# Kernel tuning notes

Hardware: AMD Instinct MI355X
Metric: run time of the kernel (lower is better)

## Reference

```python
import jax, jax.numpy as jnp
import numpy as np

B, C, H_IMG, W_IMG = 16, 384, 56, 56
NUM_HEADS = 6
HEAD_DIM = C // NUM_HEADS
BN_EPS = 1e-5


def _bn(x, gamma, beta, mean, var):
    # x: [b, ch, n] or [b, ch, h, w]; per-channel affine normalization (eval-mode BatchNorm)
    shape = (1, -1) + (1,) * (x.ndim - 2)
    scale = (gamma / jnp.sqrt(var + BN_EPS)).reshape(shape)
    shift = (beta - mean * gamma / jnp.sqrt(var + BN_EPS)).reshape(shape)
    return x * scale + shift


def setup_inputs() -> dict:
    key = jax.random.key(0)
    ks = jax.random.split(key, 12)
    c2 = 2 * C
    return {
        "x": jax.random.normal(ks[0], (B, C, H_IMG, W_IMG), jnp.float32),
        "qk_w": jax.random.normal(ks[1], (c2, C // 2), jnp.float32) * 0.05,
        "qk_gamma": jax.random.uniform(ks[2], (c2,), jnp.float32, 0.5, 1.5),
        "qk_beta": jax.random.normal(ks[3], (c2,), jnp.float32) * 0.1,
        "qk_mean": jax.random.normal(ks[4], (c2,), jnp.float32) * 0.1,
        "qk_var": jax.random.uniform(ks[5], (c2,), jnp.float32, 0.5, 1.5),
        "pe_w": jax.random.normal(ks[6], (C, 1, 3, 3), jnp.float32) * 0.1,
        "pe_gamma": jax.random.uniform(ks[7], (C,), jnp.float32, 0.5, 1.5),
        "pe_beta": jax.random.normal(ks[8], (C,), jnp.float32) * 0.1,
        "pe_mean": jax.random.normal(ks[9], (C,), jnp.float32) * 0.1,
        "pe_var": jax.random.uniform(ks[10], (C,), jnp.float32, 0.5, 1.5),
    }


def reference(x, qk_w, qk_gamma, qk_beta, qk_mean, qk_var,
              pe_w, pe_gamma, pe_beta, pe_mean, pe_var):
    b, c, h, w = x.shape
    n = h * w
    s = n ** (-0.5)
    nh, hd = NUM_HEADS, HEAD_DIM

    # grouped (groups=2) 1x1 conv: out channels [0:c] from input [0:c/2], [c:2c] from [c/2:c]
    xg = x.reshape(b, 2, c // 2, n)                       # [b, 2, c/2, n]
    wg = qk_w.reshape(2, c, c // 2)                       # [group, out_per_group, in_per_group]
    qk = jnp.einsum('bgin,goi->bgon', xg, wg).reshape(b, 2 * c, n)
    qk = _bn(qk, qk_gamma, qk_beta, qk_mean, qk_var)
    qk = jax.nn.elu(qk) + 1.0

    qk = qk.reshape(b, 2, nh, hd, n)
    q, k = qk[:, 0], qk[:, 1]                             # [b, H, d, n]
    v = x.reshape(b, nh, hd, n)                           # [b, H, d, n]

    # kv = (k*s) @ (v^T * s): [b, H, d, d]
    kv = jnp.einsum('bhdn,bhen->bhde', k * s, v * s)
    # numerator: q^T @ kv -> [b, H, n, d]
    num = jnp.einsum('bhdn,bhde->bhne', q, kv)
    # denominator: q^T @ mean_n(k) -> [b, H, n]
    den = jnp.einsum('bhdn,bhd->bhn', q, k.mean(axis=-1)) + 1e-6
    attn = (num / den[..., None]).transpose(0, 1, 3, 2).reshape(b, c, h, w)

    # depthwise 3x3 conv positional encoding on v (= x) + BN
    pe = jax.lax.conv_general_dilated(
        x, pe_w, window_strides=(1, 1), padding=((1, 1), (1, 1)),
        feature_group_count=c, dimension_numbers=('NCHW', 'OIHW', 'NCHW'))
    pe = _bn(pe, pe_gamma, pe_beta, pe_mean, pe_var)

    return attn + pe
```

## Files before the change

kernel.cpp:

```cpp
#include <hip/hip_runtime.h>
#include <math.h>

#define N_SP 3136
#define BN_EPS 1e-5f

typedef __attribute__((ext_vector_type(8))) short short8;
typedef __attribute__((ext_vector_type(4))) float f32x4;

#define K_SZ    (16*384*N_SP)
#define QB_OFF  (K_SZ)
#define QB_SZ   (16*384*N_SP)
#define KVP_OFF (QB_OFF + QB_SZ)
#define KVP_SZ  (16*6*7*64*80)
#define KVF_OFF (KVP_OFF + KVP_SZ)
#define KVF_SZ  (16*6*64*64)
#define KM_OFF  (KVF_OFF + KVF_SZ)
#define KM_SZ   (16*6*64)
#define WH_OFF  (KM_OFF + KM_SZ)
#define WSPLIT_N (2*384*192)
#define PWS_OFF (WH_OFF + WSPLIT_N)
#define PSH_OFF (PWS_OFF + 384*9)

#define FSWZ(n) ((((n) >> 1) ^ ((n) >> 2)) & 7)

__device__ __forceinline__ void bsplit(float f, ushort& h, ushort& l) {
    uint u = __float_as_uint(f);
    uint hr = (u + 0x7FFFu + ((u >> 16) & 1u)) >> 16;
    h = (ushort)hr;
    float fh = __uint_as_float(hr << 16);
    float fl = f - fh;
    uint v = __float_as_uint(fl);
    l = (ushort)((v + 0x7FFFu + ((v >> 16) & 1u)) >> 16);
}

__global__ __launch_bounds__(256) void p0_prep(
    const float* __restrict__ qk_w, const float* __restrict__ pe_w,
    const float* __restrict__ pgamma, const float* __restrict__ pbeta,
    const float* __restrict__ pmean, const float* __restrict__ pvar,
    ushort* __restrict__ wh, ushort* __restrict__ wl,
    float* __restrict__ pwsc, float* __restrict__ psh)
{
    int idx = blockIdx.x * 256 + threadIdx.x;
    if (idx < WSPLIT_N) {
        ushort h, l;
        bsplit(qk_w[idx], h, l);
        wh[idx] = h;
        wl[idx] = l;
    }
    if (idx < 384) {
        float sc = pgamma[idx] / sqrtf(pvar[idx] + BN_EPS);
        psh[idx] = pbeta[idx] - pmean[idx] * sc;
        #pragma unroll
        for (int q = 0; q < 9; ++q) pwsc[idx * 9 + q] = pe_w[idx * 9 + q] * sc;
    }
}

__global__ __launch_bounds__(256) void k1_qk_mfma(
    const float* __restrict__ x, const ushort* __restrict__ wh, const ushort* __restrict__ wl,
    const float* __restrict__ gamma, const float* __restrict__ beta,
    const float* __restrict__ mean, const float* __restrict__ var,
    uint* __restrict__ kq, float* __restrict__ qbuf)
{
    __shared__ __align__(16) ushort Ah[8192];
    __shared__ __align__(16) ushort Al[8192];
    __shared__ __align__(16) ushort Bh[4096];
    __shared__ __align__(16) ushort Bl[4096];

    const int bx = blockIdx.x;
    const int by = blockIdx.y;
    const int bz = blockIdx.z;
    const int b = bz >> 1, gg = bz & 1;
    const int t = threadIdx.x;
    const int lane = t & 63, wv = t >> 6;
    const int wr = wv >> 1, wc = wv & 1;
    const int lg = lane >> 4, l15 = lane & 15;

    f32x4 acc[4][2];
    #pragma unroll
    for (int m = 0; m < 4; ++m)
        #pragma unroll
        for (int nf = 0; nf < 2; ++nf)
            acc[m][nf] = (f32x4){0.f, 0.f, 0.f, 0.f};

    const float* xg = x + (size_t)(b * 384 + gg * 192) * N_SP + bx * 64;
    const ushort* whg = wh + (gg * 384 + by * 128) * 192;
    const ushort* wlg = wl + (gg * 384 + by * 128) * 192;

    for (int kt = 0; kt < 3; ++kt) {
        #pragma unroll
        for (int li = 0; li < 4; ++li) {
            int c = li * 256 + t;
            int row = c >> 3, kb = c & 7;
            int goff = row * 192 + kt * 64 + kb * 8;
            float4 vh = *(const float4*)(whg + goff);
            float4 vl = *(const float4*)(wlg + goff);
            int ch = (row * 8 + (kb ^ (row & 7))) * 8;
            *(float4*)&Ah[ch] = vh;
            *(float4*)&Al[ch] = vl;
        }
        #pragma unroll
        for (int li = 0; li < 2; ++li) {
            int idx = li * 256 + t;
            int kp = idx >> 4;
            int nq = idx & 15;
            int k0 = kp * 2;
            const float* px = xg + (size_t)(kt * 64 + k0) * N_SP + nq * 4;
            float4 v0 = *(const float4*)px;
            float4 v1 = *(const float4*)(px + N_SP);
            ushort h0[4], l0[4], h1[4], l1[4];
            float a0[4] = {v0.x, v0.y, v0.z, v0.w};
            float a1[4] = {v1.x, v1.y, v1.z, v1.w};
            #pragma unroll
            for (int i = 0; i < 4; ++i) { bsplit(a0[i], h0[i], l0[i]); bsplit(a1[i], h1[i], l1[i]); }
            int kb = k0 >> 3, ks = (k0 & 6) >> 1;
            #pragma unroll
            for (int i = 0; i < 4; ++i) {
                int n = nq * 4 + i;
                int chunk = n * 8 + (kb ^ FSWZ(n));
                ((uint*)Bh)[chunk * 4 + ks] = (uint)h0[i] | ((uint)h1[i] << 16);
                ((uint*)Bl)[chunk * 4 + ks] = (uint)l0[i] | ((uint)l1[i] << 16);
            }
        }
        __syncthreads();
        #pragma unroll
        for (int s = 0; s < 2; ++s) {
            short8 ah[4], al[4], bh[2], bl[2];
            int kb = s * 4 + lg;
            #pragma unroll
            for (int m = 0; m < 4; ++m) {
                int row = wr * 64 + m * 16 + l15;
                int ch = (row * 8 + (kb ^ (row & 7))) * 8;
                ah[m] = *(const short8*)&Ah[ch];
                al[m] = *(const short8*)&Al[ch];
            }
            #pragma unroll
            for (int nf = 0; nf < 2; ++nf) {
                int n = wc * 32 + nf * 16 + l15;
                int ch = (n * 8 + (kb ^ FSWZ(n))) * 8;
                bh[nf] = *(const short8*)&Bh[ch];
                bl[nf] = *(const short8*)&Bl[ch];
            }
            #pragma unroll
            for (int m = 0; m < 4; ++m)
                #pragma unroll
                for (int nf = 0; nf < 2; ++nf) {
                    acc[m][nf] = __builtin_amdgcn_mfma_f32_16x16x32_bf16(ah[m], bh[nf], acc[m][nf], 0, 0, 0);
                    acc[m][nf] = __builtin_amdgcn_mfma_f32_16x16x32_bf16(ah[m], bl[nf], acc[m][nf], 0, 0, 0);
                    acc[m][nf] = __builtin_amdgcn_mfma_f32_16x16x32_bf16(al[m], bh[nf], acc[m][nf], 0, 0, 0);
                }
        }
        __syncthreads();
    }

    float* scs = (float*)Bh;
    float* shs = scs + 128;
    if (t < 128) {
        int ch = gg * 384 + by * 128 + t;
        float sc = gamma[ch] / sqrtf(var[ch] + BN_EPS);
        scs[t] = sc;
        shs[t] = beta[ch] - mean[ch] * sc;
    }
    __syncthreads();

    size_t obase = ((size_t)b * 384 + by * 128) * N_SP + bx * 64 + wc * 32;
    if (gg == 0) {
        #pragma unroll
        for (int m = 0; m < 4; ++m)
            #pragma unroll
            for (int nf = 0; nf < 2; ++nf) {
                #pragma unroll
                for (int r = 0; r < 4; ++r) {
                    int orow = wr * 64 + m * 16 + lg * 4 + r;
                    float v = acc[m][nf][r] * scs[orow] + shs[orow];
                    v = v > 0.f ? v + 1.f : __expf(v);
                    qbuf[obase + (size_t)orow * N_SP + nf * 16 + l15] = v;
                }
            }
    } else {
        #pragma unroll
        for (int m = 0; m < 4; ++m)
            #pragma unroll
            for (int nf = 0; nf < 2; ++nf) {
                #pragma unroll
                for (int r = 0; r < 4; ++r) {
                    int orow = wr * 64 + m * 16 + lg * 4 + r;
                    float v = acc[m][nf][r] * scs[orow] + shs[orow];
                    v = v > 0.f ? v + 1.f : __expf(v);
                    ushort hh, ll;
                    bsplit(v, hh, ll);
                    kq[obase + (size_t)orow * N_SP + nf * 16 + l15] = (uint)hh | ((uint)ll << 16);
                }
            }
    }
}

__global__ __launch_bounds__(256) void k2_kv_mfma(
    const float* __restrict__ x, const uint* __restrict__ kq,
    float* __restrict__ kv_part)
{
    __shared__ __align__(16) ushort Kh[4096], Kl[4096];
    __shared__ __align__(16) ushort Vh[5120], Vl[5120];

    const int chunk = blockIdx.x;
    const int h = blockIdx.y, b = blockIdx.z;
    const int t = threadIdx.x;
    const int lane = t & 63, wv = t >> 6;
    const int lg = lane >> 4, l15 = lane & 15;

    const uint* kp  = kq + (size_t)(b*384 + h*64) * N_SP;
    const float* vp = x  + (size_t)(b*384 + h*64) * N_SP;

    #pragma unroll
    for (int li = 0; li < 4; ++li) {
        int idx = li * 256 + t;
        int row = 64 + (idx >> 6), col = idx & 63;
        int off = (row * 8 + ((col >> 3) ^ (row & 7))) * 8 + (col & 7);
        Vh[off] = (row == 64) ? (ushort)0x3F80 : (ushort)0;
        Vl[off] = 0;
    }

    f32x4 acc[5];
    #pragma unroll
    for (int nf = 0; nf < 5; ++nf) acc[nf] = (f32x4){0.f, 0.f, 0.f, 0.f};

    for (int sub = 0; sub < 7; ++sub) {
        int n0 = chunk * 448 + sub * 64;
        #pragma unroll
        for (int li = 0; li < 4; ++li) {
            int idx = li * 256 + t;
            int row = idx >> 4, sc = idx & 15;
            int off = (row * 8 + ((sc >> 1) ^ (row & 7))) * 8 + (sc & 1) * 4;
            uint4 kf = *(const uint4*)&kp[(size_t)row * N_SP + n0 + sc * 4];
            ((uint*)&Kh[off])[0] = (kf.x & 0xFFFFu) | (kf.y << 16);
            ((uint*)&Kh[off])[1] = (kf.z & 0xFFFFu) | (kf.w << 16);
            ((uint*)&Kl[off])[0] = (kf.x >> 16) | (kf.y & 0xFFFF0000u);
            ((uint*)&Kl[off])[1] = (kf.z >> 16) | (kf.w & 0xFFFF0000u);
            float4 vf = *(const float4*)&vp[(size_t)row * N_SP + n0 + sc * 4];
            ushort h0,h1,h2,h3,l0,l1,l2,l3;
            bsplit(vf.x,h0,l0); bsplit(vf.y,h1,l1); bsplit(vf.z,h2,l2); bsplit(vf.w,h3,l3);
            ((uint*)&Vh[off])[0] = (uint)h0 | ((uint)h1 << 16);
            ((uint*)&Vh[off])[1] = (uint)h2 | ((uint)h3 << 16);
            ((uint*)&Vl[off])[0] = (uint)l0 | ((uint)l1 << 16);
            ((uint*)&Vl[off])[1] = (uint)l2 | ((uint)l3 << 16);
        }
        __syncthreads();
        #pragma unroll
        for (int s = 0; s < 2; ++s) {
            int arow = wv * 16 + l15;
            int akb = (s * 4 + lg) ^ (arow & 7);
            short8 ah = *(const short8*)&Kh[(arow * 8 + akb) * 8];
            short8 al = *(const short8*)&Kl[(arow * 8 + akb) * 8];
            #pragma unroll
            for (int nf = 0; nf < 5; ++nf) {
                int brow = nf * 16 + l15;
                int bkb = (s * 4 + lg) ^ (brow & 7);
                short8 bh = *(const short8*)&Vh[(brow * 8 + bkb) * 8];
                short8 bl = *(const short8*)&Vl[(brow * 8 + bkb) * 8];
                acc[nf] = __builtin_amdgcn_mfma_f32_16x16x32_bf16(ah, bh, acc[nf], 0, 0, 0);
                acc[nf] = __builtin_amdgcn_mfma_f32_16x16x32_bf16(ah, bl, acc[nf], 0, 0, 0);
                acc[nf] = __builtin_amdgcn_mfma_f32_16x16x32_bf16(al, bh, acc[nf], 0, 0, 0);
            }
        }
        __syncthreads();
    }

    size_t base = (size_t)((b*6 + h)*7 + chunk) * 64 * 80;
    #pragma unroll
    for (int nf = 0; nf < 5; ++nf)
        #pragma unroll
        for (int r = 0; r < 4; ++r) {
            int d = wv * 16 + lg * 4 + r;
            kv_part[base + (size_t)d * 80 + nf * 16 + l15] = acc[nf][r];
        }
}

__global__ __launch_bounds__(256) void k2b_reduce(
    const float* __restrict__ kv_part,
    float* __restrict__ kvf, float* __restrict__ km)
{
    const int bh = blockIdx.x;
    const int t = threadIdx.x;
    const float inv_n = 1.0f / (float)N_SP;
    const float* base = kv_part + (size_t)bh * 7 * 5120;
    float s[20];
    #pragma unroll
    for (int j = 0; j < 20; ++j) s[j] = 0.f;
    for (int c = 0; c < 7; ++c) {
        #pragma unroll
        for (int j = 0; j < 20; ++j) s[j] += base[c * 5120 + j * 256 + t];
    }
    #pragma unroll
    for (int j = 0; j < 20; ++j) {
        int i = j * 256 + t;
        int d = i / 80, e = i % 80;
        float v = s[j] * inv_n;
        if (e < 64)       kvf[(size_t)bh * 4096 + d * 64 + e] = v;
        else if (e == 64) km[bh * 64 + d] = v;
    }
}

__global__ __launch_bounds__(256) void k3_attn_pe(
    const float* __restrict__ x, const float* __restrict__ qbuf,
    const float* __restrict__ kvf, const float* __restrict__ km,
    const float* __restrict__ pwsc, const float* __restrict__ psh,
    float* __restrict__ out)
{
    __shared__ float qs[64][68];
    __shared__ float kms[64];
    const int bx = blockIdx.x;
    const int h = blockIdx.y, b = blockIdx.z;
    const int t = threadIdx.x, tx = t & 15, ty = t >> 4;
    const int n0 = bx * 64;
    const float* qp  = qbuf + (size_t)(b * 384 + h * 64) * N_SP;
    const float* kvp = kvf + (size_t)(b * 6 + h) * 4096;
    #pragma unroll
    for (int l = 0; l < 4; ++l) {
        int idx = t + l * 256;
        int d = idx >> 4, c = idx & 15;
        *(float4*)&qs[d][c * 4] = *(const float4*)&qp[(size_t)d * N_SP + n0 + c * 4];
    }
    if (t < 64) kms[t] = km[(b * 6 + h) * 64 + t];
    __syncthreads();

    float acc[4][4] = {};
    float den[4] = {};
    #pragma unroll 8
    for (int d = 0; d < 64; ++d) {
        float4 qn = *(const float4*)&qs[d][tx * 4];
        float4 ke = *(const float4*)&kvp[d * 64 + ty * 4];
        float qq[4] = {qn.x, qn.y, qn.z, qn.w}, kk[4] = {ke.x, ke.y, ke.z, ke.w};
        float kmd = kms[d];
        #pragma unroll
        for (int p = 0; p < 4; ++p) {
            den[p] += qq[p] * kmd;
            #pragma unroll
            for (int j = 0; j < 4; ++j) acc[p][j] += qq[p] * kk[j];
        }
    }

    const int p0 = n0 + tx * 4;
    const int y = p0 / 56, xc = p0 % 56;
    #pragma unroll
    for (int j = 0; j < 4; ++j) {
        int c = h * 64 + ty * 4 + j;
        const float* xp = x + ((size_t)b * 384 + c) * N_SP;
        float s6[3][6];
        #pragma unroll
        for (int dy = 0; dy < 3; ++dy) {
            int yy = y + dy - 1;
            bool yok = (yy >= 0) && (yy < 56);
            float4 mid = make_float4(0.f, 0.f, 0.f, 0.f);
            float lf = 0.f, rt = 0.f;
            if (yok) {
                const float* xr = xp + yy * 56;
                mid = *(const float4*)&xr[xc];
                if (xc > 0)  lf = xr[xc - 1];
                if (xc < 52) rt = xr[xc + 4];
            }
            s6[dy][0] = lf;  s6[dy][1] = mid.x; s6[dy][2] = mid.y;
            s6[dy][3] = mid.z; s6[dy][4] = mid.w; s6[dy][5] = rt;
        }
        float w9[9];
        #pragma unroll
        for (int q = 0; q < 9; ++q) w9[q] = pwsc[c * 9 + q];
        float sh2 = psh[c];
        float4 r;
        float* pr = (float*)&r;
        #pragma unroll
        for (int p = 0; p < 4; ++p) {
            float conv = 0.f;
            #pragma unroll
            for (int dy = 0; dy < 3; ++dy)
                #pragma unroll
                for (int dx = 0; dx < 3; ++dx)
                    conv += w9[dy * 3 + dx] * s6[dy][p + dx];
            pr[p] = acc[p][j] / (den[p] + 1e-6f) + conv + sh2;
        }
        *(float4*)&out[((size_t)b * 384 + c) * N_SP + p0] = r;
    }
}

extern "C" void kernel_launch(void* const* d_in, const int* in_sizes, int n_in,
                              void* d_out, int out_size, void* d_ws, size_t ws_size,
                              hipStream_t stream)
{
    const float* x        = (const float*)d_in[0];
    const float* qk_w     = (const float*)d_in[1];
    const float* qk_gamma = (const float*)d_in[2];
    const float* qk_beta  = (const float*)d_in[3];
    const float* qk_mean  = (const float*)d_in[4];
    const float* qk_var   = (const float*)d_in[5];
    const float* pe_w     = (const float*)d_in[6];
    const float* pe_gamma = (const float*)d_in[7];
    const float* pe_beta  = (const float*)d_in[8];
    const float* pe_mean  = (const float*)d_in[9];
    const float* pe_var   = (const float*)d_in[10];
    float* out = (float*)d_out;

    float* ws      = (float*)d_ws;
    uint* kq       = (uint*)ws;
    float* qbuf    = ws + QB_OFF;
    float* kv_part = ws + KVP_OFF;
    float* kvf     = ws + KVF_OFF;
    float* km      = ws + KM_OFF;
    ushort* whp    = (ushort*)(ws + WH_OFF);
    ushort* wlp    = whp + WSPLIT_N;
    float* pwsc    = ws + PWS_OFF;
    float* psh     = ws + PSH_OFF;

    hipLaunchKernelGGL(p0_prep, dim3((WSPLIT_N + 255)/256), dim3(256), 0, stream,
                       qk_w, pe_w, pe_gamma, pe_beta, pe_mean, pe_var,
                       whp, wlp, pwsc, psh);
    dim3 g1(49, 3, 32);
    hipLaunchKernelGGL(k1_qk_mfma, g1, dim3(256), 0, stream,
                       x, whp, wlp, qk_gamma, qk_beta, qk_mean, qk_var, kq, qbuf);
    dim3 g2(7, 6, 16);
    hipLaunchKernelGGL(k2_kv_mfma, g2, dim3(256), 0, stream, x, kq, kv_part);
    hipLaunchKernelGGL(k2b_reduce, dim3(96), dim3(256), 0, stream,
                       kv_part, kvf, km);
    dim3 g3(49, 6, 16);
    hipLaunchKernelGGL(k3_attn_pe, g3, dim3(256), 0, stream,
                       x, qbuf, kvf, km, pwsc, psh, out);
}
```

Measured before the change: 213.3 us.

## Pre-tile QK weights into MFMA fragment layout and load directly from global

The prep kernel now stores the bf16 hi/lo weight split in a fragment-major layout, so the QK projection kernel reads A operands straight from global/L2 instead of staging them through LDS. The tile grows to 192 output rows per block (3x4 fragments per wave), which halves redundant x conversions across the y grid, and BN scales are computed before the loop. The attention+PE kernel hoists the centre-row x loads ahead of the matmul loop to overlap their latency, and both kernels get occupancy hints in launch bounds. The risks are higher register pressure and global-load latency on the A operand with no LDS reuse.

```diff
diff --git a/kernel.cpp b/kernel.cpp
--- a/kernel.cpp
+++ b/kernel.cpp
@@ -18,6 +18,7 @@
 #define KM_SZ   (16*6*64)
 #define WH_OFF  (KM_OFF + KM_SZ)
 #define WSPLIT_N (2*384*192)
+#define WF_G    (384*192)
 #define PWS_OFF (WH_OFF + WSPLIT_N)
 #define PSH_OFF (PWS_OFF + 384*9)
 
@@ -37,15 +38,19 @@
     const float* __restrict__ qk_w, const float* __restrict__ pe_w,
     const float* __restrict__ pgamma, const float* __restrict__ pbeta,
     const float* __restrict__ pmean, const float* __restrict__ pvar,
-    ushort* __restrict__ wh, ushort* __restrict__ wl,
+    ushort* __restrict__ wfh, ushort* __restrict__ wfl,
     float* __restrict__ pwsc, float* __restrict__ psh)
 {
     int idx = blockIdx.x * 256 + threadIdx.x;
     if (idx < WSPLIT_N) {
+        int g = (idx >= WF_G) ? 1 : 0;
+        int rem = idx - g * WF_G;
+        int row = rem / 192, k = rem % 192;
         ushort h, l;
         bsplit(qk_w[idx], h, l);
-        wh[idx] = h;
-        wl[idx] = l;
+        int dst = g * WF_G + ((row >> 4) * 24 + (k >> 3)) * 128 + (row & 15) * 8 + (k & 7);
+        wfh[dst] = h;
+        wfl[dst] = l;
     }
     if (idx < 384) {
         float sc = pgamma[idx] / sqrtf(pvar[idx] + BN_EPS);
@@ -55,16 +60,15 @@
     }
 }
 
-__global__ __launch_bounds__(256) void k1_qk_mfma(
-    const float* __restrict__ x, const ushort* __restrict__ wh, const ushort* __restrict__ wl,
+__global__ __launch_bounds__(256, 4) void k1_qk_mfma(
+    const float* __restrict__ x, const ushort* __restrict__ wfh, const ushort* __restrict__ wfl,
     const float* __restrict__ gamma, const float* __restrict__ beta,
     const float* __restrict__ mean, const float* __restrict__ var,
     uint* __restrict__ kq, float* __restrict__ qbuf)
 {
-    __shared__ __align__(16) ushort Ah[8192];
-    __shared__ __align__(16) ushort Al[8192];
     __shared__ __align__(16) ushort Bh[4096];
     __shared__ __align__(16) ushort Bl[4096];
+    __shared__ float scs[192], shs[192];
 
     const int bx = blockIdx.x;
     const int by = blockIdx.y;
@@ -72,32 +76,27 @@
     const int b = bz >> 1, gg = bz & 1;
     const int t = threadIdx.x;
     const int lane = t & 63, wv = t >> 6;
-    const int wr = wv >> 1, wc = wv & 1;
     const int lg = lane >> 4, l15 = lane & 15;
 
-    f32x4 acc[4][2];
-    #pragma unroll
-    for (int m = 0; m < 4; ++m)
-        #pragma unroll
-        for (int nf = 0; nf < 2; ++nf)
-            acc[m][nf] = (f32x4){0.f, 0.f, 0.f, 0.f};
+    f32x4 acc[3][4];
+    #pragma unroll
+    for (int mf = 0; mf < 3; ++mf)
+        #pragma unroll
+        for (int nf = 0; nf < 4; ++nf)
+            acc[mf][nf] = (f32x4){0.f, 0.f, 0.f, 0.f};
 
     const float* xg = x + (size_t)(b * 384 + gg * 192) * N_SP + bx * 64;
-    const ushort* whg = wh + (gg * 384 + by * 128) * 192;
-    const ushort* wlg = wl + (gg * 384 + by * 128) * 192;
+    const ushort* wfbh = wfh + gg * WF_G;
+    const ushort* wfbl = wfl + gg * WF_G;
+
+    for (int i = t; i < 192; i += 256) {
+        int ch = gg * 384 + by * 192 + i;
+        float sc = gamma[ch] / sqrtf(var[ch] + BN_EPS);
+        scs[i] = sc;
+        shs[i] = beta[ch] - mean[ch] * sc;
+    }
 
     for (int kt = 0; kt < 3; ++kt) {
-        #pragma unroll
-        for (int li = 0; li < 4; ++li) {
-            int c = li * 256 + t;
-            int row = c >> 3, kb = c & 7;
-            int goff = row * 192 + kt * 64 + kb * 8;
-            float4 vh = *(const float4*)(whg + goff);
-            float4 vl = *(const float4*)(wlg + goff);
-            int ch = (row * 8 + (kb ^ (row & 7))) * 8;
-            *(float4*)&Ah[ch] = vh;
-            *(float4*)&Al[ch] = vl;
-        }
         #pragma unroll
         for (int li = 0; li < 2; ++li) {
             int idx = li * 256 + t;
@@ -112,7 +111,7 @@
             float a1[4] = {v1.x, v1.y, v1.z, v1.w};
             #pragma unroll
             for (int i = 0; i < 4; ++i) { bsplit(a0[i], h0[i], l0[i]); bsplit(a1[i], h1[i], l1[i]); }
-            int kb = k0 >> 3, ks = (k0 & 6) >> 1;
+            int kb = k0 >> 3, ks = kp & 3;
             #pragma unroll
             for (int i = 0; i < 4; ++i) {
                 int n = nq * 4 + i;
@@ -124,71 +123,60 @@
         __syncthreads();
         #pragma unroll
         for (int s = 0; s < 2; ++s) {
-            short8 ah[4], al[4], bh[2], bl[2];
-            int kb = s * 4 + lg;
-            #pragma unroll
-            for (int m = 0; m < 4; ++m) {
-                int row = wr * 64 + m * 16 + l15;
-                int ch = (row * 8 + (kb ^ (row & 7))) * 8;
-                ah[m] = *(const short8*)&Ah[ch];
-                al[m] = *(const short8*)&Al[ch];
-            }
-            #pragma unroll
-            for (int nf = 0; nf < 2; ++nf) {
-                int n = wc * 32 + nf * 16 + l15;
-                int ch = (n * 8 + (kb ^ FSWZ(n))) * 8;
-                bh[nf] = *(const short8*)&Bh[ch];
-                bl[nf] = *(const short8*)&Bl[ch];
-            }
-            #pragma unroll
-            for (int m = 0; m < 4; ++m)
+            int kbq = s * 4 + lg;
+            int kglob = kt * 8 + kbq;
+            short8 bh[4], bl[4];
+            #pragma unroll
+            for (int nf = 0; nf < 4; ++nf) {
+                int n = nf * 16 + l15;
+                int chunk = n * 8 + (kbq ^ FSWZ(n));
+                bh[nf] = *(const short8*)&Bh[chunk * 8];
+                bl[nf] = *(const short8*)&Bl[chunk * 8];
+            }
+            #pragma unroll
+            for (int mf = 0; mf < 3; ++mf) {
+                int rb = by * 12 + wv * 3 + mf;
+                int off = (rb * 24 + kglob) * 128 + l15 * 8;
+                short8 ah = *(const short8*)&wfbh[off];
+                short8 al = *(const short8*)&wfbl[off];
                 #pragma unroll
-                for (int nf = 0; nf < 2; ++nf) {
-                    acc[m][nf] = __builtin_amdgcn_mfma_f32_16x16x32_bf16(ah[m], bh[nf], acc[m][nf], 0, 0, 0);
-                    acc[m][nf] = __builtin_amdgcn_mfma_f32_16x16x32_bf16(ah[m], bl[nf], acc[m][nf], 0, 0, 0);
-                    acc[m][nf] = __builtin_amdgcn_mfma_f32_16x16x32_bf16(al[m], bh[nf], acc[m][nf], 0, 0, 0);
+                for (int nf = 0; nf < 4; ++nf) {
+                    acc[mf][nf] = __builtin_amdgcn_mfma_f32_16x16x32_bf16(ah, bh[nf], acc[mf][nf], 0, 0, 0);
+                    acc[mf][nf] = __builtin_amdgcn_mfma_f32_16x16x32_bf16(ah, bl[nf], acc[mf][nf], 0, 0, 0);
+                    acc[mf][nf] = __builtin_amdgcn_mfma_f32_16x16x32_bf16(al, bh[nf], acc[mf][nf], 0, 0, 0);
                 }
+            }
         }
         __syncthreads();
     }
 
-    float* scs = (float*)Bh;
-    float* shs = scs + 128;
-    if (t < 128) {
-        int ch = gg * 384 + by * 128 + t;
-        float sc = gamma[ch] / sqrtf(var[ch] + BN_EPS);
-        scs[t] = sc;
-        shs[t] = beta[ch] - mean[ch] * sc;
-    }
-    __syncthreads();
-
-    size_t obase = ((size_t)b * 384 + by * 128) * N_SP + bx * 64 + wc * 32;
+    size_t obase = ((size_t)b * 384 + by * 192) * N_SP + bx * 64;
     if (gg == 0) {
         #pragma unroll
-        for (int m = 0; m < 4; ++m)
-            #pragma unroll
-            for (int nf = 0; nf < 2; ++nf) {
+        for (int mf = 0; mf < 3; ++mf)
+            #pragma unroll
+            for (int nf = 0; nf < 4; ++nf) {
                 #pragma unroll
                 for (int r = 0; r < 4; ++r) {
-                    int orow = wr * 64 + m * 16 + lg * 4 + r;
-                    float v = acc[m][nf][r] * scs[orow] + shs[orow];
+                    int lrow = wv * 48 + mf * 16 + lg * 4 + r;
+                    float v = acc[mf][nf][r] * scs[lrow] + shs[lrow];
                     v = v > 0.f ? v + 1.f : __expf(v);
-                    qbuf[obase + (size_t)orow * N_SP + nf * 16 + l15] = v;
+                    qbuf[obase + (size_t)lrow * N_SP + nf * 16 + l15] = v;
                 }
             }
     } else {
         #pragma unroll
-        for (int m = 0; m < 4; ++m)
-            #pragma unroll
-            for (int nf = 0; nf < 2; ++nf) {
+        for (int mf = 0; mf < 3; ++mf)
+            #pragma unroll
+            for (int nf = 0; nf < 4; ++nf) {
                 #pragma unroll
                 for (int r = 0; r < 4; ++r) {
-                    int orow = wr * 64 + m * 16 + lg * 4 + r;
-                    float v = acc[m][nf][r] * scs[orow] + shs[orow];
+                    int lrow = wv * 48 + mf * 16 + lg * 4 + r;
+                    float v = acc[mf][nf][r] * scs[lrow] + shs[lrow];
                     v = v > 0.f ? v + 1.f : __expf(v);
                     ushort hh, ll;
                     bsplit(v, hh, ll);
-                    kq[obase + (size_t)orow * N_SP + nf * 16 + l15] = (uint)hh | ((uint)ll << 16);
+                    kq[obase + (size_t)lrow * N_SP + nf * 16 + l15] = (uint)hh | ((uint)ll << 16);
                 }
             }
     }
@@ -299,7 +287,7 @@
     }
 }
 
-__global__ __launch_bounds__(256) void k3_attn_pe(
+__global__ __launch_bounds__(256, 4) void k3_attn_pe(
     const float* __restrict__ x, const float* __restrict__ qbuf,
     const float* __restrict__ kvf, const float* __restrict__ km,
     const float* __restrict__ pwsc, const float* __restrict__ psh,
@@ -320,6 +308,22 @@
         *(float4*)&qs[d][c * 4] = *(const float4*)&qp[(size_t)d * N_SP + n0 + c * 4];
     }
     if (t < 64) kms[t] = km[(b * 6 + h) * 64 + t];
+
+    const int p0 = n0 + tx * 4;
+    const int y = p0 / 56, xc = p0 % 56;
+    float4 mid[4][3];
+    #pragma unroll
+    for (int j = 0; j < 4; ++j) {
+        int c = h * 64 + ty * 4 + j;
+        const float* xp = x + ((size_t)b * 384 + c) * N_SP;
+        #pragma unroll
+        for (int dy = 0; dy < 3; ++dy) {
+            int yy = y + dy - 1;
+            bool yok = (yy >= 0) && (yy < 56);
+            mid[j][dy] = yok ? *(const float4*)&xp[yy * 56 + xc]
+                             : make_float4(0.f, 0.f, 0.f, 0.f);
+        }
+    }
     __syncthreads();
 
     float acc[4][4] = {};
@@ -338,8 +342,6 @@
         }
     }
 
-    const int p0 = n0 + tx * 4;
-    const int y = p0 / 56, xc = p0 % 56;
     #pragma unroll
     for (int j = 0; j < 4; ++j) {
         int c = h * 64 + ty * 4 + j;
@@ -349,16 +351,16 @@
         for (int dy = 0; dy < 3; ++dy) {
             int yy = y + dy - 1;
             bool yok = (yy >= 0) && (yy < 56);
-            float4 mid = make_float4(0.f, 0.f, 0.f, 0.f);
             float lf = 0.f, rt = 0.f;
             if (yok) {
                 const float* xr = xp + yy * 56;
-                mid = *(const float4*)&xr[xc];
                 if (xc > 0)  lf = xr[xc - 1];
                 if (xc < 52) rt = xr[xc + 4];
             }
-            s6[dy][0] = lf;  s6[dy][1] = mid.x; s6[dy][2] = mid.y;
-            s6[dy][3] = mid.z; s6[dy][4] = mid.w; s6[dy][5] = rt;
+            s6[dy][0] = lf;
+            s6[dy][1] = mid[j][dy].x; s6[dy][2] = mid[j][dy].y;
+            s6[dy][3] = mid[j][dy].z; s6[dy][4] = mid[j][dy].w;
+            s6[dy][5] = rt;
         }
         float w9[9];
         #pragma unroll
@@ -403,17 +405,17 @@
     float* kv_part = ws + KVP_OFF;
     float* kvf     = ws + KVF_OFF;
     float* km      = ws + KM_OFF;
-    ushort* whp    = (ushort*)(ws + WH_OFF);
-    ushort* wlp    = whp + WSPLIT_N;
+    ushort* wfh    = (ushort*)(ws + WH_OFF);
+    ushort* wfl    = wfh + WSPLIT_N;
     float* pwsc    = ws + PWS_OFF;
     float* psh     = ws + PSH_OFF;
 
     hipLaunchKernelGGL(p0_prep, dim3((WSPLIT_N + 255)/256), dim3(256), 0, stream,
                        qk_w, pe_w, pe_gamma, pe_beta, pe_mean, pe_var,
-                       whp, wlp, pwsc, psh);
-    dim3 g1(49, 3, 32);
+                       wfh, wfl, pwsc, psh);
+    dim3 g1(49, 2, 32);
     hipLaunchKernelGGL(k1_qk_mfma, g1, dim3(256), 0, stream,
-                       x, whp, wlp, qk_gamma, qk_beta, qk_mean, qk_var, kq, qbuf);
+                       x, wfh, wfl, qk_gamma, qk_beta, qk_mean, qk_var, kq, qbuf);
     dim3 g2(7, 6, 16);
     hipLaunchKernelGGL(k2_kv_mfma, g2, dim3(256), 0, stream, x, kq, kv_part);
     hipLaunchKernelGGL(k2b_reduce, dim3(96), dim3(256), 0, stream,
```

After: 286.1 us. 1.34x slower.
